# Kernel optimization log

Measured on AMD Instinct MI355X. Metric: run time of the kernel, lower is better.

## Reference

```python
import jax, jax.numpy as jnp
import numpy as np

N = 50000      # num_nodes
E = 800000     # num_edges (before self-loops)
IN = 512       # in_channels
HID = 64       # hidden_channels
H = 8          # num_heads (layer 1)
OUT = 128      # out_channels
NEG_SLOPE = 0.2


def setup_inputs() -> dict:
    key = jax.random.key(0)
    ks = jax.random.split(key, 10)
    x = jax.random.normal(ks[0], (N, IN), jnp.float32)
    edge_index = jax.random.randint(ks[1], (2, E), 0, N, jnp.int32)

    def glorot(k, shape):
        fan_in, fan_out = shape[0], int(np.prod(shape[1:]))
        s = jnp.sqrt(2.0 / (fan_in + fan_out)).astype(jnp.float32)
        return jax.random.normal(k, shape, jnp.float32) * s

    # layer 1: GATConv(IN -> HID, heads=H, concat=True)
    W1 = glorot(ks[2], (IN, H * HID))
    att_src1 = glorot(ks[3], (H, HID))
    att_dst1 = glorot(ks[4], (H, HID))
    b1 = jnp.zeros((H * HID,), jnp.float32)
    # layer 2: GATConv(H*HID -> OUT, heads=1, concat=False)
    W2 = glorot(ks[5], (H * HID, OUT))
    att_src2 = glorot(ks[6], (1, OUT))
    att_dst2 = glorot(ks[7], (1, OUT))
    b2 = jnp.zeros((OUT,), jnp.float32)
    return {"x": x, "edge_index": edge_index,
            "W1": W1, "b1": b1, "att_src1": att_src1, "att_dst1": att_dst1,
            "W2": W2, "b2": b2, "att_src2": att_src2, "att_dst2": att_dst2}


def gat_layer(x, src, dst, W, b, a_src, a_dst, heads, concat):
    n = x.shape[0]
    h = (x @ W).reshape(n, heads, -1)                     # [N, H, C]
    e_src = (h * a_src).sum(-1)                           # [N, H]
    e_dst = (h * a_dst).sum(-1)                           # [N, H]
    e = jax.nn.leaky_relu(e_src[src] + e_dst[dst], NEG_SLOPE)   # [E, H]
    # segment softmax over incoming edges of each destination node
    m = jax.ops.segment_max(e, dst, num_segments=n)       # [N, H]
    m = jnp.where(jnp.isneginf(m), 0.0, m)                # empty segments
    p = jnp.exp(e - m[dst])                               # [E, H]
    s = jax.ops.segment_sum(p, dst, num_segments=n)       # [N, H]
    alpha = p / (s[dst] + 1e-16)                          # [E, H]
    out = jax.ops.segment_sum(alpha[..., None] * h[src], dst, num_segments=n)  # [N, H, C]
    if concat:
        return out.reshape(n, -1) + b
    return out.mean(axis=1) + b


def reference(x, edge_index, W1, b1, att_src1, att_dst1, W2, b2, att_src2, att_dst2):
    # PyG GATConv adds self-loops by default
    loops = jnp.arange(N, dtype=edge_index.dtype)
    src = jnp.concatenate([edge_index[0], loops])
    dst = jnp.concatenate([edge_index[1], loops])
    h = gat_layer(x, src, dst, W1, b1, att_src1, att_dst1, H, True)   # [N, H*HID]
    h = jax.nn.relu(h)
    out = gat_layer(h, src, dst, W2, b2, att_src2, att_dst2, 1, False)  # [N, OUT]
    return out
```

## Files before the change

kernel.cpp:

```cpp
#include <hip/hip_runtime.h>
#include <hip/hip_fp16.h>

#define NNODES 50000
#define NEDGES 800000
#define ETOT   (NNODES + NEDGES)
#define NH     8
#define HID    64
#define D1     512
#define INC    512
#define OUTC   128
#define NEG    0.2f
#define MPAD   50048

typedef __attribute__((ext_vector_type(8))) short short8;
typedef __attribute__((ext_vector_type(4))) float f32x4;
typedef _Float16 half8v __attribute__((ext_vector_type(8)));
typedef _Float16 half2v __attribute__((ext_vector_type(2)));

__device__ __forceinline__ ushort f2h_bits(float x) {
    _Float16 h = (_Float16)x; return __builtin_bit_cast(ushort, h);
}
__device__ __forceinline__ float h2f(ushort b) {
    return (float)__builtin_bit_cast(_Float16, b);
}
__device__ __forceinline__ uint splat_h2(float p) {
    uint b = (uint)f2h_bits(p); return b | (b << 16);
}
__device__ __forceinline__ half2v as_h2(uint u) { return __builtin_bit_cast(half2v, u); }
__device__ __forceinline__ float leaky(float v) { return v >= 0.f ? v : NEG * v; }

__global__ void count_deg(const int* __restrict__ ei, int* __restrict__ deg) {
    int i = blockIdx.x * 256 + threadIdx.x;
    if (i >= ETOT) return;
    int dst = (i < NEDGES) ? ei[NEDGES + i] : (i - NEDGES);
    atomicAdd(&deg[dst], 1);
}

__global__ void scan_deg(const int* __restrict__ deg, int* __restrict__ rs) {
    __shared__ int part[1024];
    const int n = NNODES;
    const int CH = (n + 1023) / 1024;
    int t = threadIdx.x;
    int lo = t * CH, hi = min(lo + CH, n);
    int s = 0;
    for (int i = lo; i < hi; ++i) s += deg[i];
    part[t] = s;
    __syncthreads();
    for (int off = 1; off < 1024; off <<= 1) {
        int v = (t >= off) ? part[t - off] : 0;
        __syncthreads();
        part[t] += v;
        __syncthreads();
    }
    int run = (t == 0) ? 0 : part[t - 1];
    for (int i = lo; i < hi; ++i) { rs[i] = run; run += deg[i]; }
    if (hi == n) rs[n] = run;
}

__global__ void scatter_edges(const int* __restrict__ ei, int* __restrict__ cursor,
                              int* __restrict__ csr_src) {
    int i = blockIdx.x * 256 + threadIdx.x;
    if (i >= ETOT) return;
    int src, dst;
    if (i < NEDGES) { src = ei[i]; dst = ei[NEDGES + i]; }
    else            { src = dst = i - NEDGES; }
    int pos = atomicAdd(&cursor[dst], 1);
    csr_src[pos] = src;
}

__global__ void cast_f16(const float* __restrict__ x, ushort* __restrict__ xh, int n4) {
    int i = blockIdx.x * 256 + threadIdx.x;
    if (i >= n4) return;
    float4 v = *(const float4*)&x[(size_t)i * 4];
    ushort4 o = { f2h_bits(v.x), f2h_bits(v.y), f2h_bits(v.z), f2h_bits(v.w) };
    *(ushort4*)&xh[(size_t)i * 4] = o;
}

__global__ void cast_wT(const float* __restrict__ W, ushort* __restrict__ WT, int K, int N) {
    int idx = blockIdx.x * 256 + threadIdx.x;
    if (idx >= K * N) return;
    int n = idx / K, k = idx - n * K;
    WT[idx] = f2h_bits(W[(size_t)k * N + n]);
}

template<int KDIM>
__global__ __launch_bounds__(256) void gemm_f16(const ushort* __restrict__ A,
                                                const ushort* __restrict__ Bt,
                                                ushort* __restrict__ C,
                                                int M, int N) {
    __shared__ __align__(16) ushort Asl[128 * 64];
    __shared__ __align__(16) ushort Bsl[128 * 64];
    const int tid  = threadIdx.x;
    const int lane = tid & 63;
    const int wid  = tid >> 6;
    const int wr   = wid >> 1, wc = wid & 1;
    const int fr   = lane & 15, fq = lane >> 4;
    const int m0   = blockIdx.x * 128;
    const int n0   = blockIdx.y * 128;

    f32x4 acc[4][4] = {};

    const int gcol = (((lane & 7) ^ ((lane >> 3) & 7))) * 8;

    for (int k0 = 0; k0 < KDIM; k0 += 64) {
        __syncthreads();
        #pragma unroll
        for (int i = 0; i < 4; ++i) {
            int chunk = wid * 4 + i;
            int r = chunk * 8 + (lane >> 3);
            const ushort* ga = A  + (size_t)(m0 + r) * KDIM + k0 + gcol;
            const ushort* gb = Bt + (size_t)(n0 + r) * KDIM + k0 + gcol;
            __builtin_amdgcn_global_load_lds(
                (const __attribute__((address_space(1))) void*)ga,
                (__attribute__((address_space(3))) void*)(Asl + chunk * 512), 16, 0, 0);
            __builtin_amdgcn_global_load_lds(
                (const __attribute__((address_space(1))) void*)gb,
                (__attribute__((address_space(3))) void*)(Bsl + chunk * 512), 16, 0, 0);
        }
        __syncthreads();
        #pragma unroll
        for (int ks = 0; ks < 2; ++ks) {
            short8 a[4], b[4];
            #pragma unroll
            for (int m = 0; m < 4; ++m) {
                int row = wr * 64 + m * 16 + fr;
                int slot = (ks * 4 + fq) ^ (fr & 7);
                a[m] = *(const short8*)&Asl[row * 64 + slot * 8];
            }
            #pragma unroll
            for (int n = 0; n < 4; ++n) {
                int row = wc * 64 + n * 16 + fr;
                int slot = (ks * 4 + fq) ^ (fr & 7);
                b[n] = *(const short8*)&Bsl[row * 64 + slot * 8];
            }
            #pragma unroll
            for (int m = 0; m < 4; ++m)
                #pragma unroll
                for (int n = 0; n < 4; ++n)
                    acc[m][n] = __builtin_amdgcn_mfma_f32_16x16x32_f16(
                        __builtin_bit_cast(half8v, a[m]),
                        __builtin_bit_cast(half8v, b[n]), acc[m][n], 0, 0, 0);
        }
    }
    #pragma unroll
    for (int m = 0; m < 4; ++m) {
        #pragma unroll
        for (int r = 0; r < 4; ++r) {
            int row = m0 + wr * 64 + m * 16 + fq * 4 + r;
            if (row >= M) continue;
            #pragma unroll
            for (int n = 0; n < 4; ++n)
                C[(size_t)row * N + n0 + wc * 64 + n * 16 + fr] = f2h_bits(acc[m][n][r]);
        }
    }
}

__global__ void dots1(const ushort* __restrict__ h1, const float* __restrict__ a_src,
                      const float* __restrict__ a_dst,
                      float* __restrict__ es, float* __restrict__ ed) {
    int gw   = (blockIdx.x * blockDim.x + threadIdx.x) >> 6;
    int lane = threadIdx.x & 63;
    if (gw >= NNODES) return;
    short8 v = *(const short8*)&h1[(size_t)gw * D1 + lane * 8];
    half8v hv = __builtin_bit_cast(half8v, v);
    int h = lane >> 3, c0 = (lane & 7) * 8;
    float s = 0.f, d = 0.f;
    #pragma unroll
    for (int j = 0; j < 8; ++j) {
        float x = (float)hv[j];
        s += x * a_src[h * HID + c0 + j];
        d += x * a_dst[h * HID + c0 + j];
    }
    #pragma unroll
    for (int off = 1; off < 8; off <<= 1) {
        s += __shfl_xor(s, off);
        d += __shfl_xor(d, off);
    }
    if ((lane & 7) == 0) { es[gw * NH + h] = s; ed[gw * NH + h] = d; }
}

__global__ void dots2(const ushort* __restrict__ h2, const float* __restrict__ a_src,
                      const float* __restrict__ a_dst,
                      float* __restrict__ es, float* __restrict__ ed) {
    int gw   = (blockIdx.x * blockDim.x + threadIdx.x) >> 6;
    int lane = threadIdx.x & 63;
    if (gw >= NNODES) return;
    uint u = *(const uint*)&h2[(size_t)gw * OUTC + lane * 2];
    float x0 = h2f((ushort)(u & 0xffffu)), x1 = h2f((ushort)(u >> 16));
    float s = x0 * a_src[lane * 2] + x1 * a_src[lane * 2 + 1];
    float d = x0 * a_dst[lane * 2] + x1 * a_dst[lane * 2 + 1];
    #pragma unroll
    for (int off = 1; off < 64; off <<= 1) {
        s += __shfl_xor(s, off);
        d += __shfl_xor(d, off);
    }
    if (lane == 0) { es[gw] = s; ed[gw] = d; }
}

#define CAP1 128
__global__ __launch_bounds__(256) void attn1(const ushort* __restrict__ h1,
                                             const float* __restrict__ esrc,
                                             const float* __restrict__ edst,
                                             const int* __restrict__ rs,
                                             const int* __restrict__ csr_src,
                                             const float* __restrict__ b1,
                                             ushort* __restrict__ out1) {
    int t = threadIdx.x, lane = t & 63, w = t >> 6;
    int n = blockIdx.x * 4 + w;
    int beg = rs[n], deg = rs[n + 1] - beg;
    int dcap = min(deg, CAP1);
    __shared__ uint  alpha_sh[4][CAP1][9];
    __shared__ int   ssrc_sh[4][CAP1];
    uint (*alpha)[9] = alpha_sh[w];
    int* ss = ssrc_sh[w];

    for (int e = lane; e < dcap; e += 64) ss[e] = csr_src[beg + e];

    float4 edA = *(const float4*)&edst[n * NH];
    float4 edB = *(const float4*)&edst[n * NH + 4];
    float mx[8], sm[8];
    #pragma unroll
    for (int h = 0; h < 8; ++h) { mx[h] = -1e30f; sm[h] = 0.f; }

    for (int e = lane; e < deg; e += 64) {
        int s = (e < CAP1) ? ss[e] : csr_src[beg + e];
        float4 eA = *(const float4*)&esrc[(size_t)s * NH];
        float4 eB = *(const float4*)&esrc[(size_t)s * NH + 4];
        float v[8] = { leaky(eA.x + edA.x), leaky(eA.y + edA.y),
                       leaky(eA.z + edA.z), leaky(eA.w + edA.w),
                       leaky(eB.x + edB.x), leaky(eB.y + edB.y),
                       leaky(eB.z + edB.z), leaky(eB.w + edB.w) };
        #pragma unroll
        for (int h = 0; h < 8; ++h) {
            if (e < CAP1) alpha[e][h] = __float_as_uint(v[h]);
            mx[h] = fmaxf(mx[h], v[h]);
        }
    }
    #pragma unroll
    for (int off = 1; off < 64; off <<= 1)
        #pragma unroll
        for (int h = 0; h < 8; ++h)
            mx[h] = fmaxf(mx[h], __shfl_xor(mx[h], off));

    for (int e = lane; e < deg; e += 64) {
        float v[8];
        if (e < CAP1) {
            #pragma unroll
            for (int h = 0; h < 8; ++h) v[h] = __uint_as_float(alpha[e][h]);
        } else {
            int s = csr_src[beg + e];
            float4 eA = *(const float4*)&esrc[(size_t)s * NH];
            float4 eB = *(const float4*)&esrc[(size_t)s * NH + 4];
            v[0] = leaky(eA.x + edA.x); v[1] = leaky(eA.y + edA.y);
            v[2] = leaky(eA.z + edA.z); v[3] = leaky(eA.w + edA.w);
            v[4] = leaky(eB.x + edB.x); v[5] = leaky(eB.y + edB.y);
            v[6] = leaky(eB.z + edB.z); v[7] = leaky(eB.w + edB.w);
        }
        #pragma unroll
        for (int h = 0; h < 8; ++h) {
            float p = __expf(v[h] - mx[h]);
            if (e < CAP1) alpha[e][h] = splat_h2(p);
            sm[h] += p;
        }
    }
    #pragma unroll
    for (int off = 1; off < 64; off <<= 1)
        #pragma unroll
        for (int h = 0; h < 8; ++h)
            sm[h] += __shfl_xor(sm[h], off);

    int h = lane >> 3;
    float mm = mx[0], ssv = sm[0], edn = edA.x;
    float edv[8] = { edA.x, edA.y, edA.z, edA.w, edB.x, edB.y, edB.z, edB.w };
    #pragma unroll
    for (int hh = 1; hh < 8; ++hh)
        if (h == hh) { mm = mx[hh]; ssv = sm[hh]; edn = edv[hh]; }
    float ri = 1.f / (ssv + 1e-16f);

    int c0 = lane * 8;
    half2v aA0 = {}, aA1 = {}, aA2 = {}, aA3 = {};
    half2v aB0 = {}, aB1 = {}, aB2 = {}, aB3 = {};
    int e = 0;
    for (; e + 2 <= dcap; e += 2) {
        int s0i = ss[e], s1i = ss[e + 1];
        uint4 u0 = *(const uint4*)&h1[(size_t)s0i * D1 + c0];
        uint4 u1 = *(const uint4*)&h1[(size_t)s1i * D1 + c0];
        half2v p0 = as_h2(alpha[e][h]);
        half2v p1 = as_h2(alpha[e + 1][h]);
        aA0 = as_h2(u0.x) * p0 + aA0; aA1 = as_h2(u0.y) * p0 + aA1;
        aA2 = as_h2(u0.z) * p0 + aA2; aA3 = as_h2(u0.w) * p0 + aA3;
        aB0 = as_h2(u1.x) * p1 + aB0; aB1 = as_h2(u1.y) * p1 + aB1;
        aB2 = as_h2(u1.z) * p1 + aB2; aB3 = as_h2(u1.w) * p1 + aB3;
    }
    for (; e < dcap; ++e) {
        int s = ss[e];
        uint4 u = *(const uint4*)&h1[(size_t)s * D1 + c0];
        half2v p = as_h2(alpha[e][h]);
        aA0 = as_h2(u.x) * p + aA0; aA1 = as_h2(u.y) * p + aA1;
        aA2 = as_h2(u.z) * p + aA2; aA3 = as_h2(u.w) * p + aA3;
    }
    for (; e < deg; ++e) {
        int s = csr_src[beg + e];
        float p = __expf(leaky(esrc[(size_t)s * NH + h] + edn) - mm);
        half2v ph = as_h2(splat_h2(p));
        uint4 u = *(const uint4*)&h1[(size_t)s * D1 + c0];
        aA0 = as_h2(u.x) * ph + aA0; aA1 = as_h2(u.y) * ph + aA1;
        aA2 = as_h2(u.z) * ph + aA2; aA3 = as_h2(u.w) * ph + aA3;
    }
    float4 bb0 = *(const float4*)&b1[c0];
    float4 bb1 = *(const float4*)&b1[c0 + 4];
    float o0 = fmaxf(((float)aA0[0] + (float)aB0[0]) * ri + bb0.x, 0.f);
    float o1 = fmaxf(((float)aA0[1] + (float)aB0[1]) * ri + bb0.y, 0.f);
    float o2 = fmaxf(((float)aA1[0] + (float)aB1[0]) * ri + bb0.z, 0.f);
    float o3 = fmaxf(((float)aA1[1] + (float)aB1[1]) * ri + bb0.w, 0.f);
    float o4 = fmaxf(((float)aA2[0] + (float)aB2[0]) * ri + bb1.x, 0.f);
    float o5 = fmaxf(((float)aA2[1] + (float)aB2[1]) * ri + bb1.y, 0.f);
    float o6 = fmaxf(((float)aA3[0] + (float)aB3[0]) * ri + bb1.z, 0.f);
    float o7 = fmaxf(((float)aA3[1] + (float)aB3[1]) * ri + bb1.w, 0.f);
    uint4 pk;
    pk.x = (uint)f2h_bits(o0) | ((uint)f2h_bits(o1) << 16);
    pk.y = (uint)f2h_bits(o2) | ((uint)f2h_bits(o3) << 16);
    pk.z = (uint)f2h_bits(o4) | ((uint)f2h_bits(o5) << 16);
    pk.w = (uint)f2h_bits(o6) | ((uint)f2h_bits(o7) << 16);
    *(uint4*)&out1[(size_t)n * D1 + c0] = pk;
}

#define CAP2 128
__global__ __launch_bounds__(256) void attn2(const ushort* __restrict__ h2,
                                             const float* __restrict__ esrc,
                                             const float* __restrict__ edst,
                                             const int* __restrict__ rs,
                                             const int* __restrict__ csr_src,
                                             const float* __restrict__ b2,
                                             float* __restrict__ out) {
    int t = threadIdx.x;
    int g = t >> 5, lane32 = t & 31;
    int n = blockIdx.x * 8 + g;
    if (n >= NNODES) return;
    int beg = rs[n], deg = rs[n + 1] - beg;
    int dcap = min(deg, CAP2);
    __shared__ float al_sh[8][CAP2];
    __shared__ int   ss_sh[8][CAP2];
    float* al = al_sh[g];
    int*   ss = ss_sh[g];

    for (int e = lane32; e < dcap; e += 32) ss[e] = csr_src[beg + e];

    float edn = edst[n];
    float m = -1e30f;
    for (int e = lane32; e < deg; e += 32) {
        int s = (e < CAP2) ? ss[e] : csr_src[beg + e];
        float v = leaky(esrc[s] + edn);
        if (e < CAP2) al[e] = v;
        m = fmaxf(m, v);
    }
    #pragma unroll
    for (int off = 16; off; off >>= 1) m = fmaxf(m, __shfl_xor(m, off));
    float ssum = 0.f;
    for (int e = lane32; e < deg; e += 32) {
        float v = (e < CAP2) ? al[e] : leaky(esrc[csr_src[beg + e]] + edn);
        float p = __expf(v - m);
        if (e < CAP2) *(uint*)&al[e] = splat_h2(p);
        ssum += p;
    }
    #pragma unroll
    for (int off = 16; off; off >>= 1) ssum += __shfl_xor(ssum, off);
    float ri = 1.f / (ssum + 1e-16f);

    int c0 = lane32 * 4;
    half2v a01 = {}, a01b = {}, a23 = {}, a23b = {};
    int e = 0;
    for (; e + 4 <= dcap; e += 4) {
        int s0i = ss[e], s1i = ss[e + 1], s2i = ss[e + 2], s3i = ss[e + 3];
        uint2 u0 = *(const uint2*)&h2[(size_t)s0i * OUTC + c0];
        uint2 u1 = *(const uint2*)&h2[(size_t)s1i * OUTC + c0];
        uint2 u2 = *(const uint2*)&h2[(size_t)s2i * OUTC + c0];
        uint2 u3 = *(const uint2*)&h2[(size_t)s3i * OUTC + c0];
        half2v p0 = as_h2(*(const uint*)&al[e]);
        half2v p1 = as_h2(*(const uint*)&al[e + 1]);
        half2v p2 = as_h2(*(const uint*)&al[e + 2]);
        half2v p3 = as_h2(*(const uint*)&al[e + 3]);
        a01  = as_h2(u0.x) * p0 + a01;  a23  = as_h2(u0.y) * p0 + a23;
        a01b = as_h2(u1.x) * p1 + a01b; a23b = as_h2(u1.y) * p1 + a23b;
        a01  = as_h2(u2.x) * p2 + a01;  a23  = as_h2(u2.y) * p2 + a23;
        a01b = as_h2(u3.x) * p3 + a01b; a23b = as_h2(u3.y) * p3 + a23b;
    }
    for (; e < dcap; ++e) {
        int s = ss[e];
        uint2 u = *(const uint2*)&h2[(size_t)s * OUTC + c0];
        half2v p = as_h2(*(const uint*)&al[e]);
        a01 = as_h2(u.x) * p + a01;
        a23 = as_h2(u.y) * p + a23;
    }
    for (; e < deg; ++e) {
        int s = csr_src[beg + e];
        float p = __expf(leaky(esrc[s] + edn) - m);
        half2v ph = as_h2(splat_h2(p));
        uint2 u = *(const uint2*)&h2[(size_t)s * OUTC + c0];
        a01 = as_h2(u.x) * ph + a01;
        a23 = as_h2(u.y) * ph + a23;
    }
    float4 bb = *(const float4*)&b2[c0];
    float4 o;
    o.x = ((float)a01[0] + (float)a01b[0]) * ri + bb.x;
    o.y = ((float)a01[1] + (float)a01b[1]) * ri + bb.y;
    o.z = ((float)a23[0] + (float)a23b[0]) * ri + bb.z;
    o.w = ((float)a23[1] + (float)a23b[1]) * ri + bb.w;
    *(float4*)&out[(size_t)n * OUTC + c0] = o;
}

extern "C" void kernel_launch(void* const* d_in, const int* in_sizes, int n_in,
                              void* d_out, int out_size, void* d_ws, size_t ws_size,
                              hipStream_t stream) {
    const float* x   = (const float*)d_in[0];
    const int*   ei  = (const int*)  d_in[1];
    const float* W1  = (const float*)d_in[2];
    const float* b1  = (const float*)d_in[3];
    const float* as1 = (const float*)d_in[4];
    const float* ad1 = (const float*)d_in[5];
    const float* W2  = (const float*)d_in[6];
    const float* b2  = (const float*)d_in[7];
    const float* as2 = (const float*)d_in[8];
    const float* ad2 = (const float*)d_in[9];
    float* out = (float*)d_out;

    char* ws = (char*)d_ws;
    size_t off = 0;
    auto alloc = [&](size_t bytes) -> void* {
        void* p = ws + off;
        off = (off + bytes + 255) & ~(size_t)255;
        return p;
    };
    ushort* xh    = (ushort*)alloc((size_t)MPAD * INC * 2);
    ushort* w1t   = (ushort*)alloc((size_t)D1 * INC * 2);
    ushort* w2t   = (ushort*)alloc((size_t)OUTC * D1 * 2);
    ushort* h1h   = (ushort*)alloc((size_t)MPAD * D1 * 2);
    ushort* out1h = (ushort*)alloc((size_t)MPAD * D1 * 2);
    ushort* h2h   = (ushort*)alloc((size_t)MPAD * OUTC * 2);
    float*  es1   = (float*)alloc((size_t)NNODES * NH * 4);
    float*  ed1   = (float*)alloc((size_t)NNODES * NH * 4);
    float*  es2   = (float*)alloc((size_t)NNODES * 4);
    float*  ed2   = (float*)alloc((size_t)NNODES * 4);
    int*    deg   = (int*)alloc((size_t)NNODES * 4);
    int*    rs    = (int*)alloc((size_t)(NNODES + 1) * 4);
    int*    cur   = (int*)alloc((size_t)NNODES * 4);
    int*    csr   = (int*)alloc((size_t)ETOT * 4);

    hipMemsetAsync(deg, 0, (size_t)NNODES * 4, stream);
    count_deg<<<(ETOT + 255) / 256, 256, 0, stream>>>(ei, deg);
    scan_deg<<<1, 1024, 0, stream>>>(deg, rs);
    hipMemcpyAsync(cur, rs, (size_t)NNODES * 4, hipMemcpyDeviceToDevice, stream);
    scatter_edges<<<(ETOT + 255) / 256, 256, 0, stream>>>(ei, cur, csr);

    cast_f16<<<(NNODES * INC / 4 + 255) / 256, 256, 0, stream>>>(x, xh, NNODES * INC / 4);
    cast_wT<<<(INC * D1 + 255) / 256, 256, 0, stream>>>(W1, w1t, INC, D1);
    cast_wT<<<(D1 * OUTC + 255) / 256, 256, 0, stream>>>(W2, w2t, D1, OUTC);

    gemm_f16<INC><<<dim3(MPAD / 128, D1 / 128), 256, 0, stream>>>(xh, w1t, h1h, NNODES, D1);
    dots1<<<(NNODES * 64 + 255) / 256, 256, 0, stream>>>(h1h, as1, ad1, es1, ed1);
    attn1<<<NNODES / 4, 256, 0, stream>>>(h1h, es1, ed1, rs, csr, b1, out1h);

    gemm_f16<D1><<<dim3(MPAD / 128, OUTC / 128), 256, 0, stream>>>(out1h, w2t, h2h, NNODES, OUTC);
    dots2<<<(NNODES * 64 + 255) / 256, 256, 0, stream>>>(h2h, as2, ad2, es2, ed2);
    attn2<<<NNODES / 8, 256, 0, stream>>>(h2h, es2, ed2, rs, csr, b2, out);
}
```

Baseline: 590.1 us.

## Fuse layer-1 attention dots into GEMM epilogue; use 64-row tiles for layer-2 GEMM

The first GEMM now computes the per-head source and destination attention dot products from its fp32 accumulators in the epilogue, using shuffle reductions across the 16 columns of each fragment. This removes the separate dots1 kernel and its re-read of h1. The second GEMM gets its own kernel with 64-row M tiles, doubling the block count. That launch only had about 391 blocks with N=128, so the change is meant to improve occupancy. The dots are now taken from fp32 accumulators rather than fp16-rounded values, which changes the numerics slightly.

```diff
diff --git a/kernel.cpp b/kernel.cpp
--- a/kernel.cpp
+++ b/kernel.cpp
@@ -84,10 +84,14 @@
 }
 
 template<int KDIM>
-__global__ __launch_bounds__(256) void gemm_f16(const ushort* __restrict__ A,
-                                                const ushort* __restrict__ Bt,
-                                                ushort* __restrict__ C,
-                                                int M, int N) {
+__global__ __launch_bounds__(256) void gemm1_f16(const ushort* __restrict__ A,
+                                                 const ushort* __restrict__ Bt,
+                                                 ushort* __restrict__ C,
+                                                 const float* __restrict__ a_src,
+                                                 const float* __restrict__ a_dst,
+                                                 float* __restrict__ es,
+                                                 float* __restrict__ ed,
+                                                 int M, int N) {
     __shared__ __align__(16) ushort Asl[128 * 64];
     __shared__ __align__(16) ushort Bsl[128 * 64];
     const int tid  = threadIdx.x;
@@ -99,7 +103,6 @@
     const int n0   = blockIdx.y * 128;
 
     f32x4 acc[4][4] = {};
-
     const int gcol = (((lane & 7) ^ ((lane >> 3) & 7))) * 8;
 
     for (int k0 = 0; k0 < KDIM; k0 += 64) {
@@ -153,30 +156,116 @@
                 C[(size_t)row * N + n0 + wc * 64 + n * 16 + fr] = f2h_bits(acc[m][n][r]);
         }
     }
-}
-
-__global__ void dots1(const ushort* __restrict__ h1, const float* __restrict__ a_src,
-                      const float* __restrict__ a_dst,
-                      float* __restrict__ es, float* __restrict__ ed) {
-    int gw   = (blockIdx.x * blockDim.x + threadIdx.x) >> 6;
-    int lane = threadIdx.x & 63;
-    if (gw >= NNODES) return;
-    short8 v = *(const short8*)&h1[(size_t)gw * D1 + lane * 8];
-    half8v hv = __builtin_bit_cast(half8v, v);
-    int h = lane >> 3, c0 = (lane & 7) * 8;
-    float s = 0.f, d = 0.f;
-    #pragma unroll
-    for (int j = 0; j < 8; ++j) {
-        float x = (float)hv[j];
-        s += x * a_src[h * HID + c0 + j];
-        d += x * a_dst[h * HID + c0 + j];
-    }
-    #pragma unroll
-    for (int off = 1; off < 8; off <<= 1) {
-        s += __shfl_xor(s, off);
-        d += __shfl_xor(d, off);
-    }
-    if ((lane & 7) == 0) { es[gw * NH + h] = s; ed[gw * NH + h] = d; }
+    {
+        int h = (n0 + wc * 64) >> 6;
+        float as[4], ad[4];
+        #pragma unroll
+        for (int n = 0; n < 4; ++n) {
+            as[n] = a_src[h * HID + n * 16 + fr];
+            ad[n] = a_dst[h * HID + n * 16 + fr];
+        }
+        #pragma unroll
+        for (int m = 0; m < 4; ++m) {
+            #pragma unroll
+            for (int r = 0; r < 4; ++r) {
+                float s = 0.f, d = 0.f;
+                #pragma unroll
+                for (int n = 0; n < 4; ++n) {
+                    float v = acc[m][n][r];
+                    s += v * as[n];
+                    d += v * ad[n];
+                }
+                #pragma unroll
+                for (int off = 1; off < 16; off <<= 1) {
+                    s += __shfl_xor(s, off);
+                    d += __shfl_xor(d, off);
+                }
+                if (fr == 0) {
+                    int row = m0 + wr * 64 + m * 16 + fq * 4 + r;
+                    if (row < M) {
+                        es[row * NH + h] = s;
+                        ed[row * NH + h] = d;
+                    }
+                }
+            }
+        }
+    }
+}
+
+template<int KDIM>
+__global__ __launch_bounds__(256) void gemm2_f16(const ushort* __restrict__ A,
+                                                 const ushort* __restrict__ Bt,
+                                                 ushort* __restrict__ C,
+                                                 int M, int N) {
+    __shared__ __align__(16) ushort Asl[64 * 64];
+    __shared__ __align__(16) ushort Bsl[128 * 64];
+    const int tid  = threadIdx.x;
+    const int lane = tid & 63;
+    const int wid  = tid >> 6;
+    const int wr   = wid >> 1, wc = wid & 1;
+    const int fr   = lane & 15, fq = lane >> 4;
+    const int m0   = blockIdx.x * 64;
+    const int n0   = blockIdx.y * 128;
+
+    f32x4 acc[2][4] = {};
+    const int gcol = (((lane & 7) ^ ((lane >> 3) & 7))) * 8;
+
+    for (int k0 = 0; k0 < KDIM; k0 += 64) {
+        __syncthreads();
+        #pragma unroll
+        for (int i = 0; i < 2; ++i) {
+            int chunk = wid * 2 + i;
+            int r = chunk * 8 + (lane >> 3);
+            const ushort* ga = A + (size_t)(m0 + r) * KDIM + k0 + gcol;
+            __builtin_amdgcn_global_load_lds(
+                (const __attribute__((address_space(1))) void*)ga,
+                (__attribute__((address_space(3))) void*)(Asl + chunk * 512), 16, 0, 0);
+        }
+        #pragma unroll
+        for (int i = 0; i < 4; ++i) {
+            int chunk = wid * 4 + i;
+            int r = chunk * 8 + (lane >> 3);
+            const ushort* gb = Bt + (size_t)(n0 + r) * KDIM + k0 + gcol;
+            __builtin_amdgcn_global_load_lds(
+                (const __attribute__((address_space(1))) void*)gb,
+                (__attribute__((address_space(3))) void*)(Bsl + chunk * 512), 16, 0, 0);
+        }
+        __syncthreads();
+        #pragma unroll
+        for (int ks = 0; ks < 2; ++ks) {
+            short8 a[2], b[4];
+            #pragma unroll
+            for (int m = 0; m < 2; ++m) {
+                int row = wr * 32 + m * 16 + fr;
+                int slot = (ks * 4 + fq) ^ (fr & 7);
+                a[m] = *(const short8*)&Asl[row * 64 + slot * 8];
+            }
+            #pragma unroll
+            for (int n = 0; n < 4; ++n) {
+                int row = wc * 64 + n * 16 + fr;
+                int slot = (ks * 4 + fq) ^ (fr & 7);
+                b[n] = *(const short8*)&Bsl[row * 64 + slot * 8];
+            }
+            #pragma unroll
+            for (int m = 0; m < 2; ++m)
+                #pragma unroll
+                for (int n = 0; n < 4; ++n)
+                    acc[m][n] = __builtin_amdgcn_mfma_f32_16x16x32_f16(
+                        __builtin_bit_cast(half8v, a[m]),
+                        __builtin_bit_cast(half8v, b[n]), acc[m][n], 0, 0, 0);
+        }
+    }
+    #pragma unroll
+    for (int m = 0; m < 2; ++m) {
+        #pragma unroll
+        for (int r = 0; r < 4; ++r) {
+            int row = m0 + wr * 32 + m * 16 + fq * 4 + r;
+            if (row >= M) continue;
+            #pragma unroll
+            for (int n = 0; n < 4; ++n)
+                C[(size_t)row * N + n0 + wc * 64 + n * 16 + fr] = f2h_bits(acc[m][n][r]);
+        }
+    }
 }
 
 __global__ void dots2(const ushort* __restrict__ h2, const float* __restrict__ a_src,
@@ -456,11 +545,11 @@
     cast_wT<<<(INC * D1 + 255) / 256, 256, 0, stream>>>(W1, w1t, INC, D1);
     cast_wT<<<(D1 * OUTC + 255) / 256, 256, 0, stream>>>(W2, w2t, D1, OUTC);
 
-    gemm_f16<INC><<<dim3(MPAD / 128, D1 / 128), 256, 0, stream>>>(xh, w1t, h1h, NNODES, D1);
-    dots1<<<(NNODES * 64 + 255) / 256, 256, 0, stream>>>(h1h, as1, ad1, es1, ed1);
+    gemm1_f16<INC><<<dim3(MPAD / 128, D1 / 128), 256, 0, stream>>>(
+        xh, w1t, h1h, as1, ad1, es1, ed1, NNODES, D1);
     attn1<<<NNODES / 4, 256, 0, stream>>>(h1h, es1, ed1, rs, csr, b1, out1h);
 
-    gemm_f16<D1><<<dim3(MPAD / 128, OUTC / 128), 256, 0, stream>>>(out1h, w2t, h2h, NNODES, OUTC);
+    gemm2_f16<D1><<<dim3(MPAD / 64, OUTC / 128), 256, 0, stream>>>(out1h, w2t, h2h, NNODES, OUTC);
     dots2<<<(NNODES * 64 + 255) / 256, 256, 0, stream>>>(h2h, as2, ad2, es2, ed2);
     attn2<<<NNODES / 8, 256, 0, stream>>>(h2h, es2, ed2, rs, csr, b2, out);
 }
```

Result: no change. 596.1 us (+1.0%).
